# Performance work log

Hardware: AMD Instinct MI355X
Metric: run time of the kernel (lower is better)

## Reference

```python
import jax, jax.numpy as jnp
import numpy as np

# Production-scale detection head dims
B_TOTAL = 16      # num_tbins(4) * batch_size(4)
NUM_ANCHORS = 100000
NUM_CLASSES = 8


def setup_inputs() -> dict:
    key = jax.random.key(0)
    k1, k2, k3, k4 = jax.random.split(key, 4)
    # anchors [A,4] = (cx, cy, w, h); widths/heights strictly positive
    ctr = jax.random.uniform(k1, (NUM_ANCHORS, 2), jnp.float32) * 512.0
    wh = jax.random.uniform(k2, (NUM_ANCHORS, 2), jnp.float32) * 64.0 + 8.0
    anchors = jnp.concatenate([ctr, wh], axis=-1)
    loc_preds = jax.random.normal(k3, (B_TOTAL, NUM_ANCHORS, 4), jnp.float32)
    # class scores in [0,1] (post-sigmoid semantics)
    cls_preds = jax.nn.sigmoid(jax.random.normal(k4, (B_TOTAL, NUM_ANCHORS, NUM_CLASSES), jnp.float32))
    return {
        "anchors": anchors,
        "loc_preds": loc_preds,
        "cls_preds": cls_preds,
        "varx": 0.1,
        "vary": 0.2,
        "score_thresh": 0.7,
        "batch_size": 4,
    }


def reference(anchors, loc_preds, cls_preds, varx, vary, score_thresh, batch_size):
    """Anchor decode + score-threshold filtering.

    Faithful to BoxDecoder.forward, but jit-compatible: instead of
    boolean-mask compaction into ragged per-(t,i) lists (data-dependent
    shapes), we return the dense [B*A*C, 6] box tensor plus the keep mask
    and batch_index; (mask, batch_index) fully determine the ragged
    targets[t][i] = box_tensor[mask & (batch_index == t*batch_size+i)].
    """
    B, A, C = cls_preds.shape
    # decode: xy = loc[:2]*varx*anchor_wh + anchor_xy ; wh = exp(loc[2:]*vary)*anchor_wh
    xy = loc_preds[..., :2] * varx * anchors[..., 2:] + anchors[..., :2]
    wh = jnp.exp(loc_preds[..., 2:] * vary) * anchors[..., 2:]
    box_preds = jnp.concatenate([xy - wh * 0.5, xy + wh * 0.5], axis=-1)  # [B,A,4]
    # expand boxes over classes, flatten to [B*A*C, ...] (same order as torch view(-1,...))
    boxes = jnp.broadcast_to(box_preds[:, :, None, :], (B, A, C, 4)).reshape(-1, 4)
    scores = cls_preds.reshape(-1)
    # idxs = b*C + c  ->  label = c+1, batch_index = b
    labels = jnp.broadcast_to(jnp.arange(C, dtype=jnp.float32) + 1.0, (B, A, C)).reshape(-1)
    batch_index = jnp.broadcast_to(jnp.arange(B, dtype=jnp.int32)[:, None, None], (B, A, C)).reshape(-1)
    box_tensor = jnp.concatenate([boxes, scores[:, None], labels[:, None]], axis=1)  # [B*A*C, 6]
    mask = scores >= score_thresh  # keep mask (compaction left to consumer / kernel)
    return box_tensor, mask, batch_index
```

## Files before the change

kernel.cpp:

```cpp
#include <hip/hip_runtime.h>
#include <math.h>


#define MAGIC_SHIFT 38

typedef float vfloat4 __attribute__((ext_vector_type(4)));

__global__ __launch_bounds__(256) void box_decode_coop(
    const vfloat4* __restrict__ anchors,
    const vfloat4* __restrict__ loc,
    const vfloat4* __restrict__ cls4,
    const float*   __restrict__ varx_p,
    const float*   __restrict__ vary_p,
    const float*   __restrict__ th_p,
    vfloat4*       __restrict__ out_box4,
    vfloat4*       __restrict__ out_mask4,
    vfloat4*       __restrict__ out_bidx4,
    unsigned nT, unsigned A,
    unsigned long long invA)
{
    __shared__ vfloat4 s_box[64];
    __shared__ vfloat4 s_cls4[128];
    __shared__ float   s_b[64];
    const float* s_cls = (const float*)s_cls4;

    const unsigned tid = threadIdx.x;
    const unsigned t0  = blockIdx.x * 64u;

    const float varx = *varx_p;
    const float vary = *vary_p;
    const float th   = *th_p;

    if (tid < 64u) {
        unsigned t = t0 + tid;
        if (t < nT) {
            unsigned b = (unsigned)(((unsigned long long)t * invA) >> MAGIC_SHIFT);
            unsigned a = t - b * A;
            vfloat4 anc = anchors[a];
            vfloat4 lp  = __builtin_nontemporal_load(&loc[t]);
            float x = fmaf(lp.x * varx, anc.z, anc.x);
            float y = fmaf(lp.y * varx, anc.w, anc.y);
            float w = expf(lp.z * vary) * anc.z;
            float h = expf(lp.w * vary) * anc.w;
            vfloat4 bx;
            bx.x = fmaf(w, -0.5f, x);
            bx.y = fmaf(h, -0.5f, y);
            bx.z = fmaf(w,  0.5f, x);
            bx.w = fmaf(h,  0.5f, y);
            s_box[tid] = bx;
            s_b[tid]   = (float)b;
        }
    } else if (tid < 192u) {
        unsigned i  = tid - 64u;
        unsigned gi = t0 * 2u + i;
        if (gi < nT * 2u)
            s_cls4[i] = __builtin_nontemporal_load(&cls4[gi]);
    }
    __syncthreads();

    {
        const unsigned nt_blk = (nT - t0 < 64u) ? (nT - t0) : 64u;
        const unsigned lim    = nt_blk * 12u;
        const unsigned base   = t0 * 12u;
#pragma unroll
        for (unsigned k = 0u; k < 3u; ++k) {
            unsigned lg = k * 256u + tid;
            if (lg < lim) {
                unsigned lt = lg / 12u;
                unsigned j  = lg - lt * 12u;
                unsigned s  = j / 3u;
                unsigned jm = j - s * 3u;
                vfloat4 bx  = s_box[lt];
                float sc0 = s_cls[lt * 8u + 2u * s];
                float sc1 = s_cls[lt * 8u + 2u * s + 1u];
                float l0  = (float)(2u * s + 1u);
                float l1  = (float)(2u * s + 2u);
                bool j0 = (jm == 0u);
                bool j1 = (jm == 1u);
                vfloat4 r;
                r.x = j0 ? bx.x : (j1 ? sc0  : bx.z);
                r.y = j0 ? bx.y : (j1 ? l0   : bx.w);
                r.z = j0 ? bx.z : (j1 ? bx.x : sc1);
                r.w = j0 ? bx.w : (j1 ? bx.y : l1);
                out_box4[base + lg] = r;
            }
        }
    }

    {
        const unsigned nt_blk = (nT - t0 < 64u) ? (nT - t0) : 64u;
        const unsigned lim    = nt_blk * 2u;
        const unsigned mbase  = t0 * 2u;
        if (tid < 128u) {
            unsigned i = tid;
            if (i < lim) {
                vfloat4 c = s_cls4[i];
                vfloat4 m;
                m.x = (c.x >= th) ? 1.0f : 0.0f;
                m.y = (c.y >= th) ? 1.0f : 0.0f;
                m.z = (c.z >= th) ? 1.0f : 0.0f;
                m.w = (c.w >= th) ? 1.0f : 0.0f;
                out_mask4[mbase + i] = m;
            }
        } else {
            unsigned i = tid - 128u;
            if (i < lim) {
                float bf = s_b[i >> 1];
                vfloat4 bb = {bf, bf, bf, bf};
                out_bidx4[mbase + i] = bb;
            }
        }
    }
}

__global__ __launch_bounds__(256) void box_decode_kernel(
    const float4* __restrict__ anchors,
    const float4* __restrict__ loc,
    const float*  __restrict__ cls,
    const float*  __restrict__ varx_p,
    const float*  __restrict__ vary_p,
    const float*  __restrict__ th_p,
    vfloat4*      __restrict__ out_box4,
    float*        __restrict__ out_mask,
    float*        __restrict__ out_bidx,
    unsigned n4, unsigned A, unsigned C, unsigned f4_per_t,
    unsigned long long invA, unsigned long long invF)
{
    unsigned g = blockIdx.x * 256u + threadIdx.x;
    if (g >= n4) return;
    unsigned t  = (unsigned)(((unsigned long long)g * invF) >> MAGIC_SHIFT);
    unsigned j  = g - t * f4_per_t;
    unsigned b  = (unsigned)(((unsigned long long)t * invA) >> MAGIC_SHIFT);
    unsigned a  = t - b * A;
    unsigned s  = j / 3u;
    unsigned jm = j - s * 3u;
    float varx = *varx_p, vary = *vary_p, th = *th_p;
    float4 anc = anchors[a];
    float4 lp  = loc[t];
    float x = fmaf(lp.x * varx, anc.z, anc.x);
    float y = fmaf(lp.y * varx, anc.w, anc.y);
    float w = expf(lp.z * vary) * anc.z;
    float h = expf(lp.w * vary) * anc.w;
    float x1 = fmaf(w, -0.5f, x);
    float y1 = fmaf(h, -0.5f, y);
    float x2 = fmaf(w,  0.5f, x);
    float y2 = fmaf(h,  0.5f, y);
    unsigned r0 = t * C + 2u * s;
    float bf = (float)b;
    vfloat4 r;
    if (jm == 0u) {
        r.x = x1; r.y = y1; r.z = x2; r.w = y2;
    } else if (jm == 1u) {
        float sc0 = cls[r0];
        r.x = sc0; r.y = (float)(2u * s + 1u); r.z = x1; r.w = y1;
        out_mask[r0] = (sc0 >= th) ? 1.0f : 0.0f;
        out_bidx[r0] = bf;
    } else {
        float sc1 = cls[r0 + 1u];
        r.x = x2; r.y = y2; r.z = sc1; r.w = (float)(2u * s + 2u);
        out_mask[r0 + 1u] = (sc1 >= th) ? 1.0f : 0.0f;
        out_bidx[r0 + 1u] = bf;
    }
    out_box4[g] = r;
}

extern "C" void kernel_launch(void* const* d_in, const int* in_sizes, int n_in,
                              void* d_out, int out_size, void* d_ws, size_t ws_size,
                              hipStream_t stream) {
    const float* anchors = (const float*)d_in[0];
    const float* loc     = (const float*)d_in[1];
    const float* cls     = (const float*)d_in[2];
    const float* varx_p  = (const float*)d_in[3];
    const float* vary_p  = (const float*)d_in[4];
    const float* th_p    = (const float*)d_in[5];

    unsigned A = (unsigned)(in_sizes[0] / 4);
    unsigned B = (unsigned)((unsigned)in_sizes[1] / (4u * A));
    unsigned C = (unsigned)((unsigned)in_sizes[2] / (A * B));
    unsigned nT = B * A;
    unsigned rows = nT * C;

    float* out_box  = (float*)d_out;
    float* out_mask = out_box + (size_t)rows * 6;
    float* out_bidx = out_mask + rows;

    unsigned long long invA = ((1ULL << MAGIC_SHIFT) / A) + 1ULL;

    if (C == 8u) {
        unsigned nb = (nT + 63u) / 64u;
        box_decode_coop<<<dim3(nb), dim3(256), 0, stream>>>(
            (const vfloat4*)anchors, (const vfloat4*)loc, (const vfloat4*)cls,
            varx_p, vary_p, th_p,
            (vfloat4*)out_box, (vfloat4*)out_mask, (vfloat4*)out_bidx,
            nT, A, invA);
    } else {
        unsigned f4_per_t = (6u * C) / 4u;
        unsigned n4 = rows * 6u / 4u;
        unsigned long long invF = ((1ULL << MAGIC_SHIFT) / f4_per_t) + 1ULL;
        unsigned nb = (n4 + 255u) / 256u;
        box_decode_kernel<<<dim3(nb), dim3(256), 0, stream>>>(
            (const float4*)anchors, (const float4*)loc, cls,
            varx_p, vary_p, th_p,
            (vfloat4*)out_box, out_mask, out_bidx,
            n4, A, C, f4_per_t, invA, invF);
    }
}
```

Measured before the change: 456.3 us.

## Convert box decode to persistent per-wavefront chunk loop without block barriers

New measurement: 473.0 us. +3.7%, slower.

```diff
diff --git a/kernel.cpp b/kernel.cpp
--- a/kernel.cpp
+++ b/kernel.cpp
@@ -6,7 +6,7 @@
 
 typedef float vfloat4 __attribute__((ext_vector_type(4)));
 
-__global__ __launch_bounds__(256) void box_decode_coop(
+__global__ __launch_bounds__(256) void box_decode_pers(
     const vfloat4* __restrict__ anchors,
     const vfloat4* __restrict__ loc,
     const vfloat4* __restrict__ cls4,
@@ -16,28 +16,35 @@
     vfloat4*       __restrict__ out_box4,
     vfloat4*       __restrict__ out_mask4,
     vfloat4*       __restrict__ out_bidx4,
-    unsigned nT, unsigned A,
+    unsigned nChunks, unsigned nT, unsigned A,
     unsigned long long invA)
 {
-    __shared__ vfloat4 s_box[64];
-    __shared__ vfloat4 s_cls4[128];
-    __shared__ float   s_b[64];
-    const float* s_cls = (const float*)s_cls4;
-
-    const unsigned tid = threadIdx.x;
-    const unsigned t0  = blockIdx.x * 64u;
+    __shared__ vfloat4 s_box[4][64];
+    __shared__ vfloat4 s_cls[4][128];
+
+    const unsigned wv   = threadIdx.x >> 6;
+    const unsigned lane = threadIdx.x & 63u;
+    vfloat4* sbox  = s_box[wv];
+    vfloat4* scls4 = s_cls[wv];
+    const float* scls = (const float*)scls4;
 
     const float varx = *varx_p;
     const float vary = *vary_p;
     const float th   = *th_p;
 
-    if (tid < 64u) {
-        unsigned t = t0 + tid;
-        if (t < nT) {
+    const unsigned gw = blockIdx.x * 4u + wv;
+    const unsigned nw = gridDim.x * 4u;
+
+    for (unsigned ch = gw; ch < nChunks; ch += nw) {
+        const unsigned t0     = ch * 64u;
+        const unsigned nt_blk = (nT - t0 < 64u) ? (nT - t0) : 64u;
+
+        if (lane < nt_blk) {
+            unsigned t = t0 + lane;
             unsigned b = (unsigned)(((unsigned long long)t * invA) >> MAGIC_SHIFT);
             unsigned a = t - b * A;
             vfloat4 anc = anchors[a];
-            vfloat4 lp  = __builtin_nontemporal_load(&loc[t]);
+            vfloat4 lp  = loc[t];
             float x = fmaf(lp.x * varx, anc.z, anc.x);
             float y = fmaf(lp.y * varx, anc.w, anc.y);
             float w = expf(lp.z * vary) * anc.z;
@@ -47,32 +54,60 @@
             bx.y = fmaf(h, -0.5f, y);
             bx.z = fmaf(w,  0.5f, x);
             bx.w = fmaf(h,  0.5f, y);
-            s_box[tid] = bx;
-            s_b[tid]   = (float)b;
-        }
-    } else if (tid < 192u) {
-        unsigned i  = tid - 64u;
-        unsigned gi = t0 * 2u + i;
-        if (gi < nT * 2u)
-            s_cls4[i] = __builtin_nontemporal_load(&cls4[gi]);
-    }
-    __syncthreads();
-
-    {
-        const unsigned nt_blk = (nT - t0 < 64u) ? (nT - t0) : 64u;
-        const unsigned lim    = nt_blk * 12u;
-        const unsigned base   = t0 * 12u;
+            sbox[lane] = bx;
+        }
+
+        const unsigned cbase = t0 * 2u;
+        const unsigned clim  = nt_blk * 2u;
+        if (lane < clim) {
+            vfloat4 c = cls4[cbase + lane];
+            scls4[lane] = c;
+            vfloat4 m;
+            m.x = (c.x >= th) ? 1.0f : 0.0f;
+            m.y = (c.y >= th) ? 1.0f : 0.0f;
+            m.z = (c.z >= th) ? 1.0f : 0.0f;
+            m.w = (c.w >= th) ? 1.0f : 0.0f;
+            out_mask4[cbase + lane] = m;
+            unsigned tm = t0 + (lane >> 1);
+            unsigned bm = (unsigned)(((unsigned long long)tm * invA) >> MAGIC_SHIFT);
+            float bf = (float)bm;
+            vfloat4 bb = {bf, bf, bf, bf};
+            out_bidx4[cbase + lane] = bb;
+        }
+        {
+            unsigned l2 = lane + 64u;
+            if (l2 < clim) {
+                vfloat4 c = cls4[cbase + l2];
+                scls4[l2] = c;
+                vfloat4 m;
+                m.x = (c.x >= th) ? 1.0f : 0.0f;
+                m.y = (c.y >= th) ? 1.0f : 0.0f;
+                m.z = (c.z >= th) ? 1.0f : 0.0f;
+                m.w = (c.w >= th) ? 1.0f : 0.0f;
+                out_mask4[cbase + l2] = m;
+                unsigned tm = t0 + 32u + (lane >> 1);
+                unsigned bm = (unsigned)(((unsigned long long)tm * invA) >> MAGIC_SHIFT);
+                float bf = (float)bm;
+                vfloat4 bb = {bf, bf, bf, bf};
+                out_bidx4[cbase + l2] = bb;
+            }
+        }
+
+        asm volatile("s_waitcnt lgkmcnt(0)" ::: "memory");
+
+        const unsigned lim  = nt_blk * 12u;
+        const unsigned base = t0 * 12u;
 #pragma unroll
-        for (unsigned k = 0u; k < 3u; ++k) {
-            unsigned lg = k * 256u + tid;
+        for (unsigned k = 0u; k < 12u; ++k) {
+            unsigned lg = k * 64u + lane;
             if (lg < lim) {
                 unsigned lt = lg / 12u;
                 unsigned j  = lg - lt * 12u;
                 unsigned s  = j / 3u;
                 unsigned jm = j - s * 3u;
-                vfloat4 bx  = s_box[lt];
-                float sc0 = s_cls[lt * 8u + 2u * s];
-                float sc1 = s_cls[lt * 8u + 2u * s + 1u];
+                vfloat4 bx  = sbox[lt];
+                float sc0 = scls[lt * 8u + 2u * s];
+                float sc1 = scls[lt * 8u + 2u * s + 1u];
                 float l0  = (float)(2u * s + 1u);
                 float l1  = (float)(2u * s + 2u);
                 bool j0 = (jm == 0u);
@@ -83,31 +118,6 @@
                 r.z = j0 ? bx.z : (j1 ? bx.x : sc1);
                 r.w = j0 ? bx.w : (j1 ? bx.y : l1);
                 out_box4[base + lg] = r;
-            }
-        }
-    }
-
-    {
-        const unsigned nt_blk = (nT - t0 < 64u) ? (nT - t0) : 64u;
-        const unsigned lim    = nt_blk * 2u;
-        const unsigned mbase  = t0 * 2u;
-        if (tid < 128u) {
-            unsigned i = tid;
-            if (i < lim) {
-                vfloat4 c = s_cls4[i];
-                vfloat4 m;
-                m.x = (c.x >= th) ? 1.0f : 0.0f;
-                m.y = (c.y >= th) ? 1.0f : 0.0f;
-                m.z = (c.z >= th) ? 1.0f : 0.0f;
-                m.w = (c.w >= th) ? 1.0f : 0.0f;
-                out_mask4[mbase + i] = m;
-            }
-        } else {
-            unsigned i = tid - 128u;
-            if (i < lim) {
-                float bf = s_b[i >> 1];
-                vfloat4 bb = {bf, bf, bf, bf};
-                out_bidx4[mbase + i] = bb;
             }
         }
     }
@@ -187,12 +197,14 @@
     unsigned long long invA = ((1ULL << MAGIC_SHIFT) / A) + 1ULL;
 
     if (C == 8u) {
-        unsigned nb = (nT + 63u) / 64u;
-        box_decode_coop<<<dim3(nb), dim3(256), 0, stream>>>(
+        unsigned nChunks = (nT + 63u) / 64u;
+        unsigned nb = (nChunks + 3u) / 4u;
+        if (nb > 2048u) nb = 2048u;
+        box_decode_pers<<<dim3(nb), dim3(256), 0, stream>>>(
             (const vfloat4*)anchors, (const vfloat4*)loc, (const vfloat4*)cls,
             varx_p, vary_p, th_p,
             (vfloat4*)out_box, (vfloat4*)out_mask, (vfloat4*)out_bidx,
-            nT, A, invA);
+            nChunks, nT, A, invA);
     } else {
         unsigned f4_per_t = (6u * C) / 4u;
         unsigned n4 = rows * 6u / 4u;
```
